# Kernel tuning notes

Measured on AMD Instinct MI355X. Metric: run time of the kernel, lower is better.

Reference implementation:

```python
import jax, jax.numpy as jnp
import numpy as np

TAU = 0.2  # temperature

def setup_inputs() -> dict:
    key = jax.random.key(0)
    k1, k2, k3 = jax.random.split(key, 3)
    query = jax.random.normal(k1, (8192, 128), dtype=jnp.float32)
    pos = jax.random.normal(k2, (8192, 128), dtype=jnp.float32)
    neg = jax.random.normal(k3, (16384, 128), dtype=jnp.float32)
    return {"query": query, "pos": pos, "neg": neg}

def reference(query, pos, neg):
    # scores: [N, M] = query @ neg^T / tau
    scores = jnp.einsum('nd,md->nm', query, neg) / TAU
    # positive logits: [N]
    pos_logit = jnp.sum(query * pos, axis=-1) / TAU
    # loss = mean_n( logsumexp_m(scores) - pos_logit )
    lse = jax.scipy.special.logsumexp(scores, axis=-1)
    return jnp.mean(lse - pos_logit)
```

## Files before the change

kernel.cpp:

```cpp
#include <hip/hip_runtime.h>
#include <cstdint>

#define NQ    8192
#define NNEG  16384
#define DIM   128
#define SPLIT 16
#define CHUNK (NNEG / SPLIT)
#define K_SCALE 7.2134752044448169f
#define LN2     0.69314718055994531f
#define EXP_C 8388608.0f
#define EXP_B 1065353216.0f

typedef __attribute__((ext_vector_type(8))) int   i32x8;
typedef __attribute__((ext_vector_type(4))) float f32x4;

union U8 { i32x8 v; int4 h[2]; };

__device__ inline void async_load16(const void* g, void* l) {
    __builtin_amdgcn_global_load_lds(
        (const __attribute__((address_space(1))) void*)g,
        (__attribute__((address_space(3))) void*)l, 16, 0, 0);
}

__device__ inline float waveReduceSum(float v) {
#pragma unroll
    for (int m = 32; m >= 1; m >>= 1) v += __shfl_xor(v, m, 64);
    return v;
}

__device__ inline float fexp2(float y, float t) {
    float v = fmaxf(fmaf(y, EXP_C, t), 0.0f);
    return __int_as_float((int)v);
}

__global__ __launch_bounds__(256) void iw_prep(
    const float* __restrict__ q, const float* __restrict__ p,
    const float* __restrict__ neg,
    unsigned char* __restrict__ qb8, unsigned char* __restrict__ nb8,
    float* __restrict__ out)
{
    const int tid = threadIdx.x;
    const int t = blockIdx.x * 256 + tid;
    constexpr int QT = NQ * DIM / 8;
    if (t < QT) {
        const float4* q4 = (const float4*)q;
        float4 v0 = q4[t * 2], v1 = q4[t * 2 + 1];
        int w0 = __builtin_amdgcn_cvt_pk_fp8_f32(v0.x * K_SCALE, v0.y * K_SCALE, 0, false);
        w0     = __builtin_amdgcn_cvt_pk_fp8_f32(v0.z * K_SCALE, v0.w * K_SCALE, w0, true);
        int w1 = __builtin_amdgcn_cvt_pk_fp8_f32(v1.x * K_SCALE, v1.y * K_SCALE, 0, false);
        w1     = __builtin_amdgcn_cvt_pk_fp8_f32(v1.z * K_SCALE, v1.w * K_SCALE, w1, true);
        ((int2*)qb8)[t] = make_int2(w0, w1);
        const float4* p4 = (const float4*)p;
        float4 p0 = p4[t * 2], p1 = p4[t * 2 + 1];
        float acc = fmaf(v0.x, p0.x, fmaf(v0.y, p0.y, fmaf(v0.z, p0.z, v0.w * p0.w)));
        acc = fmaf(v1.x, p1.x, fmaf(v1.y, p1.y, fmaf(v1.z, p1.z, fmaf(v1.w, p1.w, acc))));
        acc = waveReduceSum(acc);
        __shared__ float red[4];
        if ((tid & 63) == 0) red[tid >> 6] = acc;
        __syncthreads();
        if (tid == 0) {
            float s = red[0] + red[1] + red[2] + red[3];
            atomicAdd(out, s * (-1.0f / (0.2f * (float)NQ)));
        }
    } else {
        int j = t - QT;
        const float4* n4 = (const float4*)neg;
        float4 v0 = n4[j * 2], v1 = n4[j * 2 + 1];
        int w0 = __builtin_amdgcn_cvt_pk_fp8_f32(v0.x, v0.y, 0, false);
        w0     = __builtin_amdgcn_cvt_pk_fp8_f32(v0.z, v0.w, w0, true);
        int w1 = __builtin_amdgcn_cvt_pk_fp8_f32(v1.x, v1.y, 0, false);
        w1     = __builtin_amdgcn_cvt_pk_fp8_f32(v1.z, v1.w, w1, true);
        ((int2*)nb8)[j] = make_int2(w0, w1);
    }
}

__global__ __launch_bounds__(256, 4) void iw_main(
    const unsigned char* __restrict__ qb8, const unsigned char* __restrict__ nb8,
    float2* __restrict__ partial)
{
    constexpr int BM = 128, BN = 64, NIT = CHUNK / BN;
    __shared__ alignas(16) unsigned char n_lds[2 * BN * DIM];

    const int tid  = threadIdx.x;
    const int lane = tid & 63;
    const int w    = tid >> 6;
    const int quad = lane >> 4;
    const int c0   = lane & 15;

    const int row0   = blockIdx.x * BM;
    const int nbase0 = blockIdx.y * CHUNK;

    U8 afrag[2];
#pragma unroll
    for (int rs = 0; rs < 2; ++rs) {
        const int qrow = row0 + w * 32 + rs * 16 + c0;
        const int4* pa = reinterpret_cast<const int4*>(qb8 + (size_t)qrow * DIM + quad * 32);
        afrag[rs].h[0] = pa[0];
        afrag[rs].h[1] = pa[1];
    }

    int srcoff[2], dstoff[2];
#pragma unroll
    for (int j = 0; j < 2; ++j) {
        int L  = (w * 2 + j) * 64 + lane;
        int h  = L & 1, G = L >> 1;
        int r  = G >> 2;
        int kb = (G & 3) ^ (r & 3);
        srcoff[j] = r * DIM + kb * 32 + h * 16;
        dstoff[j] = (w * 2 + j) * 1024;
    }
#pragma unroll
    for (int j = 0; j < 2; ++j)
        async_load16(nb8 + (size_t)nbase0 * DIM + srcoff[j], n_lds + dstoff[j]);
    __syncthreads();

    const int bbase = ((c0 << 2) + (quad ^ (c0 & 3))) * 32;

    float m_s[2][4], l_s[2][4];
#pragma unroll
    for (int rs = 0; rs < 2; ++rs)
#pragma unroll
        for (int i = 0; i < 4; ++i) { m_s[rs][i] = -1e30f; l_s[rs][i] = 0.f; }

    const f32x4 zero4 = {0.f, 0.f, 0.f, 0.f};

    for (int it = 0; it < NIT; ++it) {
        const int buf = (it & 1) * (BN * DIM);
        if (it + 1 < NIT) {
            const unsigned char* src = nb8 + (size_t)(nbase0 + (it + 1) * BN) * DIM;
            const int nbuf = ((it + 1) & 1) * (BN * DIM);
#pragma unroll
            for (int j = 0; j < 2; ++j)
                async_load16(src + srcoff[j], n_lds + nbuf + dstoff[j]);
        }

        f32x4 acc[2][4];
#pragma unroll
        for (int ns = 0; ns < 4; ++ns) {
            const int4* pb = reinterpret_cast<const int4*>(n_lds + buf + bbase + ns * 2048);
            U8 b;
            b.h[0] = pb[0];
            b.h[1] = pb[1];
            acc[0][ns] = __builtin_amdgcn_mfma_scale_f32_16x16x128_f8f6f4(
                afrag[0].v, b.v, zero4, 0, 0, 0, 127, 0, 127);
            acc[1][ns] = __builtin_amdgcn_mfma_scale_f32_16x16x128_f8f6f4(
                afrag[1].v, b.v, zero4, 0, 0, 0, 127, 0, 127);
        }

#pragma unroll
        for (int rs = 0; rs < 2; ++rs) {
#pragma unroll
            for (int i = 0; i < 4; ++i) {
                float y0 = acc[rs][0][i], y1 = acc[rs][1][i];
                float y2 = acc[rs][2][i], y3 = acc[rs][3][i];
                float m0 = m_s[rs][i];
                float nm = fmaxf(fmaxf(fmaxf(y2, y3), m0), fmaxf(y0, y1));
                float t  = fmaf(nm, -EXP_C, EXP_B);
                float e0 = fexp2(y0, t), e1 = fexp2(y1, t);
                float e2 = fexp2(y2, t), e3 = fexp2(y3, t);
                float er = fexp2(m0, t);
                l_s[rs][i] = fmaf(l_s[rs][i], er, (e0 + e1) + (e2 + e3));
                m_s[rs][i] = nm;
            }
        }
        __syncthreads();
    }

#pragma unroll
    for (int rs = 0; rs < 2; ++rs) {
#pragma unroll
        for (int i = 0; i < 4; ++i) {
            float m = m_s[rs][i], l = l_s[rs][i];
#pragma unroll
            for (int s = 1; s < 16; s <<= 1) {
                float om = __shfl_xor(m, s, 64);
                float ol = __shfl_xor(l, s, 64);
                float nm = fmaxf(m, om);
                l = l * __builtin_amdgcn_exp2f(m - nm) + ol * __builtin_amdgcn_exp2f(om - nm);
                m = nm;
            }
            if (c0 == 0) {
                int grow = row0 + w * 32 + rs * 16 + quad * 4 + i;
                partial[(size_t)blockIdx.y * NQ + grow] = make_float2(m, l);
            }
        }
    }
}

__global__ __launch_bounds__(256) void iw_merge(
    const float2* __restrict__ partial, float* __restrict__ out)
{
    const int tid = threadIdx.x;
    const int row = blockIdx.x * 256 + tid;
    float M = -1e30f, L = 0.f;
#pragma unroll
    for (int c = 0; c < SPLIT; ++c) {
        float2 p = partial[(size_t)c * NQ + row];
        float nm = fmaxf(M, p.x);
        L = L * __builtin_amdgcn_exp2f(M - nm) + p.y * __builtin_amdgcn_exp2f(p.x - nm);
        M = nm;
    }
    float lse = LN2 * (M + __log2f(L));
    float v = lse * (1.0f / (float)NQ);
    v = waveReduceSum(v);
    __shared__ float red[4];
    if ((tid & 63) == 0) red[tid >> 6] = v;
    __syncthreads();
    if (tid == 0) atomicAdd(out, red[0] + red[1] + red[2] + red[3]);
}

extern "C" void kernel_launch(void* const* d_in, const int* in_sizes, int n_in,
                              void* d_out, int out_size, void* d_ws, size_t ws_size,
                              hipStream_t stream) {
    const float* q   = (const float*)d_in[0];
    const float* pos = (const float*)d_in[1];
    const float* neg = (const float*)d_in[2];
    float* out = (float*)d_out;

    unsigned char* qb8 = (unsigned char*)d_ws;
    unsigned char* nb8 = qb8 + (size_t)NQ * DIM;
    float2* partial    = (float2*)(nb8 + (size_t)NNEG * DIM);

    hipMemsetAsync(out, 0, sizeof(float), stream);
    iw_prep <<<1536, 256, 0, stream>>>(q, pos, neg, qb8, nb8, out);
    iw_main <<<dim3(NQ / 128, SPLIT), 256, 0, stream>>>(qb8, nb8, partial);
    iw_merge<<<32,   256, 0, stream>>>(partial, out);
}
```

Measured before the change: 112.7 us.

## Software-pipeline MFMA tiles with online-softmax update of previous tile

Restructures the main loop so the MFMA for tile i+1 is issued before the exp/logsumexp update of tile i, using two accumulator sets in a manually unrolled by-two loop. The goal is to overlap matrix-core latency with VALU exponent work instead of stalling on MFMA results each iteration. It raises register pressure (two accumulator arrays) under a 4-waves occupancy bound and hardcodes the iteration count (16 tiles).

Result: slower. 157.7 us (+39.9%).

```diff
diff --git a/kernel.cpp b/kernel.cpp
--- a/kernel.cpp
+++ b/kernel.cpp
@@ -124,20 +124,18 @@
 
     const f32x4 zero4 = {0.f, 0.f, 0.f, 0.f};
 
-    for (int it = 0; it < NIT; ++it) {
-        const int buf = (it & 1) * (BN * DIM);
-        if (it + 1 < NIT) {
-            const unsigned char* src = nb8 + (size_t)(nbase0 + (it + 1) * BN) * DIM;
-            const int nbuf = ((it + 1) & 1) * (BN * DIM);
-#pragma unroll
-            for (int j = 0; j < 2; ++j)
-                async_load16(src + srcoff[j], n_lds + nbuf + dstoff[j]);
-        }
-
-        f32x4 acc[2][4];
+    auto prefetch = [&](int it) {
+        const unsigned char* src = nb8 + (size_t)(nbase0 + it * BN) * DIM;
+        const int nbuf = (it & 1) * (BN * DIM);
+#pragma unroll
+        for (int j = 0; j < 2; ++j)
+            async_load16(src + srcoff[j], n_lds + nbuf + dstoff[j]);
+    };
+
+    auto compute_tile = [&](int bufoff, f32x4 (&acc)[2][4]) {
 #pragma unroll
         for (int ns = 0; ns < 4; ++ns) {
-            const int4* pb = reinterpret_cast<const int4*>(n_lds + buf + bbase + ns * 2048);
+            const int4* pb = reinterpret_cast<const int4*>(n_lds + bufoff + bbase + ns * 2048);
             U8 b;
             b.h[0] = pb[0];
             b.h[1] = pb[1];
@@ -146,7 +144,9 @@
             acc[1][ns] = __builtin_amdgcn_mfma_scale_f32_16x16x128_f8f6f4(
                 afrag[1].v, b.v, zero4, 0, 0, 0, 127, 0, 127);
         }
-
+    };
+
+    auto lse_update = [&](f32x4 (&acc)[2][4]) {
 #pragma unroll
         for (int rs = 0; rs < 2; ++rs) {
 #pragma unroll
@@ -163,8 +163,30 @@
                 m_s[rs][i] = nm;
             }
         }
+    };
+
+    f32x4 accA[2][4], accB[2][4];
+
+    prefetch(1);
+    compute_tile(0, accA);
+    __syncthreads();
+
+    for (int p = 0; p < 7; ++p) {
+        const int it = 1 + 2 * p;
+        prefetch(it + 1);
+        compute_tile(BN * DIM, accB);
+        lse_update(accA);
         __syncthreads();
-    }
+
+        prefetch(it + 2);
+        compute_tile(0, accA);
+        lse_update(accB);
+        __syncthreads();
+    }
+
+    compute_tile(BN * DIM, accB);
+    lse_update(accA);
+    lse_update(accB);
 
 #pragma unroll
     for (int rs = 0; rs < 2; ++rs) {
```

## Load negative fragments directly from global into registers with double buffering

Applied to the files above, without the earlier changes.

Removes the LDS staging buffer and async global-to-LDS loads for the negative tile. Each wave now loads its B fragments straight from global memory into registers, ping-ponging between two register sets across a manually unrolled loop, and the per-iteration block barrier is gone. Occupancy hint drops from 4 to 3 blocks to make room for the extra registers. The trade is less cross-wave sharing of B data, since each of the four waves fetches the same tile separately and relies on cache, and possible stalls from global latency.

Result: slower. 138.3 us (+22.7%).

```diff
diff --git a/kernel.cpp b/kernel.cpp
--- a/kernel.cpp
+++ b/kernel.cpp
@@ -15,12 +15,6 @@
 typedef __attribute__((ext_vector_type(4))) float f32x4;
 
 union U8 { i32x8 v; int4 h[2]; };
-
-__device__ inline void async_load16(const void* g, void* l) {
-    __builtin_amdgcn_global_load_lds(
-        (const __attribute__((address_space(1))) void*)g,
-        (__attribute__((address_space(3))) void*)l, 16, 0, 0);
-}
 
 __device__ inline float waveReduceSum(float v) {
 #pragma unroll
@@ -74,12 +68,11 @@
     }
 }
 
-__global__ __launch_bounds__(256, 4) void iw_main(
+__global__ __launch_bounds__(256, 3) void iw_main(
     const unsigned char* __restrict__ qb8, const unsigned char* __restrict__ nb8,
     float2* __restrict__ partial)
 {
-    constexpr int BM = 128, BN = 64, NIT = CHUNK / BN;
-    __shared__ alignas(16) unsigned char n_lds[2 * BN * DIM];
+    constexpr int BM = 128, BN = 64;
 
     const int tid  = threadIdx.x;
     const int lane = tid & 63;
@@ -99,22 +92,7 @@
         afrag[rs].h[1] = pa[1];
     }
 
-    int srcoff[2], dstoff[2];
-#pragma unroll
-    for (int j = 0; j < 2; ++j) {
-        int L  = (w * 2 + j) * 64 + lane;
-        int h  = L & 1, G = L >> 1;
-        int r  = G >> 2;
-        int kb = (G & 3) ^ (r & 3);
-        srcoff[j] = r * DIM + kb * 32 + h * 16;
-        dstoff[j] = (w * 2 + j) * 1024;
-    }
-#pragma unroll
-    for (int j = 0; j < 2; ++j)
-        async_load16(nb8 + (size_t)nbase0 * DIM + srcoff[j], n_lds + dstoff[j]);
-    __syncthreads();
-
-    const int bbase = ((c0 << 2) + (quad ^ (c0 & 3))) * 32;
+    const unsigned char* pt = nb8 + (size_t)(nbase0 + c0) * DIM + quad * 32;
 
     float m_s[2][4], l_s[2][4];
 #pragma unroll
@@ -123,48 +101,79 @@
         for (int i = 0; i < 4; ++i) { m_s[rs][i] = -1e30f; l_s[rs][i] = 0.f; }
 
     const f32x4 zero4 = {0.f, 0.f, 0.f, 0.f};
-
-    for (int it = 0; it < NIT; ++it) {
-        const int buf = (it & 1) * (BN * DIM);
-        if (it + 1 < NIT) {
-            const unsigned char* src = nb8 + (size_t)(nbase0 + (it + 1) * BN) * DIM;
-            const int nbuf = ((it + 1) & 1) * (BN * DIM);
-#pragma unroll
-            for (int j = 0; j < 2; ++j)
-                async_load16(src + srcoff[j], n_lds + nbuf + dstoff[j]);
-        }
-
-        f32x4 acc[2][4];
-#pragma unroll
-        for (int ns = 0; ns < 4; ++ns) {
-            const int4* pb = reinterpret_cast<const int4*>(n_lds + buf + bbase + ns * 2048);
-            U8 b;
-            b.h[0] = pb[0];
-            b.h[1] = pb[1];
-            acc[0][ns] = __builtin_amdgcn_mfma_scale_f32_16x16x128_f8f6f4(
-                afrag[0].v, b.v, zero4, 0, 0, 0, 127, 0, 127);
-            acc[1][ns] = __builtin_amdgcn_mfma_scale_f32_16x16x128_f8f6f4(
-                afrag[1].v, b.v, zero4, 0, 0, 0, 127, 0, 127);
-        }
-
-#pragma unroll
-        for (int rs = 0; rs < 2; ++rs) {
-#pragma unroll
-            for (int i = 0; i < 4; ++i) {
-                float y0 = acc[rs][0][i], y1 = acc[rs][1][i];
-                float y2 = acc[rs][2][i], y3 = acc[rs][3][i];
-                float m0 = m_s[rs][i];
-                float nm = fmaxf(fmaxf(fmaxf(y2, y3), m0), fmaxf(y0, y1));
-                float t  = fmaf(nm, -EXP_C, EXP_B);
-                float e0 = fexp2(y0, t), e1 = fexp2(y1, t);
-                float e2 = fexp2(y2, t), e3 = fexp2(y3, t);
-                float er = fexp2(m0, t);
-                l_s[rs][i] = fmaf(l_s[rs][i], er, (e0 + e1) + (e2 + e3));
-                m_s[rs][i] = nm;
-            }
-        }
-        __syncthreads();
-    }
+    f32x4 acc[2][4];
+    U8 bA[4], bB[4];
+
+#define LOADB(B, PT) do {                                                   \
+    const int4* _p0 = reinterpret_cast<const int4*>((PT));                  \
+    (B)[0].h[0] = _p0[0]; (B)[0].h[1] = _p0[1];                             \
+    const int4* _p1 = reinterpret_cast<const int4*>((PT) + 2048);           \
+    (B)[1].h[0] = _p1[0]; (B)[1].h[1] = _p1[1];                             \
+    const int4* _p2 = reinterpret_cast<const int4*>((PT) + 4096);           \
+    (B)[2].h[0] = _p2[0]; (B)[2].h[1] = _p2[1];                             \
+    const int4* _p3 = reinterpret_cast<const int4*>((PT) + 6144);           \
+    (B)[3].h[0] = _p3[0]; (B)[3].h[1] = _p3[1];                             \
+} while (0)
+
+#define COMPUTE(B) do {                                                     \
+    acc[0][0] = __builtin_amdgcn_mfma_scale_f32_16x16x128_f8f6f4(           \
+        afrag[0].v, (B)[0].v, zero4, 0, 0, 0, 127, 0, 127);                 \
+    acc[1][0] = __builtin_amdgcn_mfma_scale_f32_16x16x128_f8f6f4(           \
+        afrag[1].v, (B)[0].v, zero4, 0, 0, 0, 127, 0, 127);                 \
+    acc[0][1] = __builtin_amdgcn_mfma_scale_f32_16x16x128_f8f6f4(           \
+        afrag[0].v, (B)[1].v, zero4, 0, 0, 0, 127, 0, 127);                 \
+    acc[1][1] = __builtin_amdgcn_mfma_scale_f32_16x16x128_f8f6f4(           \
+        afrag[1].v, (B)[1].v, zero4, 0, 0, 0, 127, 0, 127);                 \
+    acc[0][2] = __builtin_amdgcn_mfma_scale_f32_16x16x128_f8f6f4(           \
+        afrag[0].v, (B)[2].v, zero4, 0, 0, 0, 127, 0, 127);                 \
+    acc[1][2] = __builtin_amdgcn_mfma_scale_f32_16x16x128_f8f6f4(           \
+        afrag[1].v, (B)[2].v, zero4, 0, 0, 0, 127, 0, 127);                 \
+    acc[0][3] = __builtin_amdgcn_mfma_scale_f32_16x16x128_f8f6f4(           \
+        afrag[0].v, (B)[3].v, zero4, 0, 0, 0, 127, 0, 127);                 \
+    acc[1][3] = __builtin_amdgcn_mfma_scale_f32_16x16x128_f8f6f4(           \
+        afrag[1].v, (B)[3].v, zero4, 0, 0, 0, 127, 0, 127);                 \
+} while (0)
+
+#define LSE_UPDATE() do {                                                   \
+    _Pragma("unroll")                                                       \
+    for (int rs = 0; rs < 2; ++rs) {                                        \
+        _Pragma("unroll")                                                   \
+        for (int i = 0; i < 4; ++i) {                                       \
+            float y0 = acc[rs][0][i], y1 = acc[rs][1][i];                   \
+            float y2 = acc[rs][2][i], y3 = acc[rs][3][i];                   \
+            float m0 = m_s[rs][i];                                          \
+            float nm = fmaxf(fmaxf(fmaxf(y2, y3), m0), fmaxf(y0, y1));      \
+            float tt = fmaf(nm, -EXP_C, EXP_B);                             \
+            float e0 = fexp2(y0, tt), e1 = fexp2(y1, tt);                   \
+            float e2 = fexp2(y2, tt), e3 = fexp2(y3, tt);                   \
+            float er = fexp2(m0, tt);                                       \
+            l_s[rs][i] = fmaf(l_s[rs][i], er, (e0 + e1) + (e2 + e3));       \
+            m_s[rs][i] = nm;                                                \
+        }                                                                   \
+    }                                                                       \
+} while (0)
+
+    LOADB(bA, pt);
+    pt += 8192;
+
+    for (int p = 0; p < 7; ++p) {
+        LOADB(bB, pt);  pt += 8192;
+        COMPUTE(bA);
+        LSE_UPDATE();
+        LOADB(bA, pt);  pt += 8192;
+        COMPUTE(bB);
+        LSE_UPDATE();
+    }
+
+    LOADB(bB, pt);
+    COMPUTE(bA);
+    LSE_UPDATE();
+    COMPUTE(bB);
+    LSE_UPDATE();
+
+#undef LOADB
+#undef COMPUTE
+#undef LSE_UPDATE
 
 #pragma unroll
     for (int rs = 0; rs < 2; ++rs) {
```

## Halve row tile and software-pipeline MFMA with online logsumexp update

Applied to the files above, without the earlier changes.

The query row tile per block shrinks from 128 to 64, so each wave holds one 16-row A fragment, and the grid doubles to 2048 blocks. The main loop is manually unrolled with two accumulator sets, so the MFMAs for tile t+1 are issued before the exp/max logsumexp update of tile t, overlapping matrix and vector work. Launch bounds drop from 4 to 2 waves per SIMD hint. Every negative tile is now loaded from LDS and global memory twice as often per query row, which raises load traffic, and register pressure from the two accumulator sets may cut occupancy.

Measured after the change: 111.4 us. About the same (-1.2%).

```diff
diff --git a/kernel.cpp b/kernel.cpp
--- a/kernel.cpp
+++ b/kernel.cpp
@@ -74,11 +74,11 @@
     }
 }
 
-__global__ __launch_bounds__(256, 4) void iw_main(
+__global__ __launch_bounds__(256, 2) void iw_main(
     const unsigned char* __restrict__ qb8, const unsigned char* __restrict__ nb8,
     float2* __restrict__ partial)
 {
-    constexpr int BM = 128, BN = 64, NIT = CHUNK / BN;
+    constexpr int BM = 64, BN = 64;
     __shared__ alignas(16) unsigned char n_lds[2 * BN * DIM];
 
     const int tid  = threadIdx.x;
@@ -90,13 +90,12 @@
     const int row0   = blockIdx.x * BM;
     const int nbase0 = blockIdx.y * CHUNK;
 
-    U8 afrag[2];
-#pragma unroll
-    for (int rs = 0; rs < 2; ++rs) {
-        const int qrow = row0 + w * 32 + rs * 16 + c0;
+    U8 afrag;
+    {
+        const int qrow = row0 + w * 16 + c0;
         const int4* pa = reinterpret_cast<const int4*>(qb8 + (size_t)qrow * DIM + quad * 32);
-        afrag[rs].h[0] = pa[0];
-        afrag[rs].h[1] = pa[1];
+        afrag.h[0] = pa[0];
+        afrag.h[1] = pa[1];
     }
 
     int srcoff[2], dstoff[2];
@@ -109,80 +108,101 @@
         srcoff[j] = r * DIM + kb * 32 + h * 16;
         dstoff[j] = (w * 2 + j) * 1024;
     }
-#pragma unroll
-    for (int j = 0; j < 2; ++j)
-        async_load16(nb8 + (size_t)nbase0 * DIM + srcoff[j], n_lds + dstoff[j]);
+
+    const int bbase = ((c0 << 2) + (quad ^ (c0 & 3))) * 32;
+
+    float m_s[4], l_s[4];
+#pragma unroll
+    for (int i = 0; i < 4; ++i) { m_s[i] = -1e30f; l_s[i] = 0.f; }
+
+    const f32x4 zero4 = {0.f, 0.f, 0.f, 0.f};
+    f32x4 accA[4], accB[4];
+
+#define PREFETCH(T) do {                                                    \
+    const unsigned char* _src = nb8 + (size_t)(nbase0 + (T) * BN) * DIM;    \
+    unsigned char* _dst = n_lds + ((T) & 1) * (BN * DIM);                   \
+    async_load16(_src + srcoff[0], _dst + dstoff[0]);                       \
+    async_load16(_src + srcoff[1], _dst + dstoff[1]);                       \
+} while (0)
+
+#define COMPUTE(ACC, T) do {                                                \
+    const unsigned char* _b = n_lds + ((T) & 1) * (BN * DIM) + bbase;       \
+    U8 _b0, _b1, _b2, _b3;                                                  \
+    { const int4* _p = reinterpret_cast<const int4*>(_b);                   \
+      _b0.h[0] = _p[0]; _b0.h[1] = _p[1]; }                                 \
+    { const int4* _p = reinterpret_cast<const int4*>(_b + 2048);            \
+      _b1.h[0] = _p[0]; _b1.h[1] = _p[1]; }                                 \
+    { const int4* _p = reinterpret_cast<const int4*>(_b + 4096);            \
+      _b2.h[0] = _p[0]; _b2.h[1] = _p[1]; }                                 \
+    { const int4* _p = reinterpret_cast<const int4*>(_b + 6144);            \
+      _b3.h[0] = _p[0]; _b3.h[1] = _p[1]; }                                 \
+    (ACC)[0] = __builtin_amdgcn_mfma_scale_f32_16x16x128_f8f6f4(            \
+        afrag.v, _b0.v, zero4, 0, 0, 0, 127, 0, 127);                       \
+    (ACC)[1] = __builtin_amdgcn_mfma_scale_f32_16x16x128_f8f6f4(            \
+        afrag.v, _b1.v, zero4, 0, 0, 0, 127, 0, 127);                       \
+    (ACC)[2] = __builtin_amdgcn_mfma_scale_f32_16x16x128_f8f6f4(            \
+        afrag.v, _b2.v, zero4, 0, 0, 0, 127, 0, 127);                       \
+    (ACC)[3] = __builtin_amdgcn_mfma_scale_f32_16x16x128_f8f6f4(            \
+        afrag.v, _b3.v, zero4, 0, 0, 0, 127, 0, 127);                       \
+} while (0)
+
+#define LSE_UPDATE(ACC) do {                                                \
+    _Pragma("unroll")                                                       \
+    for (int i = 0; i < 4; ++i) {                                           \
+        float y0 = (ACC)[0][i], y1 = (ACC)[1][i];                           \
+        float y2 = (ACC)[2][i], y3 = (ACC)[3][i];                           \
+        float m0 = m_s[i];                                                  \
+        float nm = fmaxf(fmaxf(fmaxf(y2, y3), m0), fmaxf(y0, y1));          \
+        float tt = fmaf(nm, -EXP_C, EXP_B);                                 \
+        float e0 = fexp2(y0, tt), e1 = fexp2(y1, tt);                       \
+        float e2 = fexp2(y2, tt), e3 = fexp2(y3, tt);                       \
+        float er = fexp2(m0, tt);                                           \
+        l_s[i] = fmaf(l_s[i], er, (e0 + e1) + (e2 + e3));                   \
+        m_s[i] = nm;                                                        \
+    }                                                                       \
+} while (0)
+
+    PREFETCH(0);
     __syncthreads();
-
-    const int bbase = ((c0 << 2) + (quad ^ (c0 & 3))) * 32;
-
-    float m_s[2][4], l_s[2][4];
-#pragma unroll
-    for (int rs = 0; rs < 2; ++rs)
-#pragma unroll
-        for (int i = 0; i < 4; ++i) { m_s[rs][i] = -1e30f; l_s[rs][i] = 0.f; }
-
-    const f32x4 zero4 = {0.f, 0.f, 0.f, 0.f};
-
-    for (int it = 0; it < NIT; ++it) {
-        const int buf = (it & 1) * (BN * DIM);
-        if (it + 1 < NIT) {
-            const unsigned char* src = nb8 + (size_t)(nbase0 + (it + 1) * BN) * DIM;
-            const int nbuf = ((it + 1) & 1) * (BN * DIM);
-#pragma unroll
-            for (int j = 0; j < 2; ++j)
-                async_load16(src + srcoff[j], n_lds + nbuf + dstoff[j]);
+    PREFETCH(1);
+    COMPUTE(accA, 0);
+    __syncthreads();
+
+    for (int p = 0; p < 7; ++p) {
+        const int t1 = 2 * p + 1;
+        PREFETCH(t1 + 1);
+        COMPUTE(accB, t1);
+        LSE_UPDATE(accA);
+        __syncthreads();
+
+        PREFETCH(t1 + 2);
+        COMPUTE(accA, t1 + 1);
+        LSE_UPDATE(accB);
+        __syncthreads();
+    }
+
+    COMPUTE(accB, 15);
+    LSE_UPDATE(accA);
+    LSE_UPDATE(accB);
+
+#undef PREFETCH
+#undef COMPUTE
+#undef LSE_UPDATE
+
+#pragma unroll
+    for (int i = 0; i < 4; ++i) {
+        float m = m_s[i], l = l_s[i];
+#pragma unroll
+        for (int s = 1; s < 16; s <<= 1) {
+            float om = __shfl_xor(m, s, 64);
+            float ol = __shfl_xor(l, s, 64);
+            float nm = fmaxf(m, om);
+            l = l * __builtin_amdgcn_exp2f(m - nm) + ol * __builtin_amdgcn_exp2f(om - nm);
+            m = nm;
         }
-
-        f32x4 acc[2][4];
-#pragma unroll
-        for (int ns = 0; ns < 4; ++ns) {
-            const int4* pb = reinterpret_cast<const int4*>(n_lds + buf + bbase + ns * 2048);
-            U8 b;
-            b.h[0] = pb[0];
-            b.h[1] = pb[1];
-            acc[0][ns] = __builtin_amdgcn_mfma_scale_f32_16x16x128_f8f6f4(
-                afrag[0].v, b.v, zero4, 0, 0, 0, 127, 0, 127);
-            acc[1][ns] = __builtin_amdgcn_mfma_scale_f32_16x16x128_f8f6f4(
-                afrag[1].v, b.v, zero4, 0, 0, 0, 127, 0, 127);
-        }
-
-#pragma unroll
-        for (int rs = 0; rs < 2; ++rs) {
-#pragma unroll
-            for (int i = 0; i < 4; ++i) {
-                float y0 = acc[rs][0][i], y1 = acc[rs][1][i];
-                float y2 = acc[rs][2][i], y3 = acc[rs][3][i];
-                float m0 = m_s[rs][i];
-                float nm = fmaxf(fmaxf(fmaxf(y2, y3), m0), fmaxf(y0, y1));
-                float t  = fmaf(nm, -EXP_C, EXP_B);
-                float e0 = fexp2(y0, t), e1 = fexp2(y1, t);
-                float e2 = fexp2(y2, t), e3 = fexp2(y3, t);
-                float er = fexp2(m0, t);
-                l_s[rs][i] = fmaf(l_s[rs][i], er, (e0 + e1) + (e2 + e3));
-                m_s[rs][i] = nm;
-            }
-        }
-        __syncthreads();
-    }
-
-#pragma unroll
-    for (int rs = 0; rs < 2; ++rs) {
-#pragma unroll
-        for (int i = 0; i < 4; ++i) {
-            float m = m_s[rs][i], l = l_s[rs][i];
-#pragma unroll
-            for (int s = 1; s < 16; s <<= 1) {
-                float om = __shfl_xor(m, s, 64);
-                float ol = __shfl_xor(l, s, 64);
-                float nm = fmaxf(m, om);
-                l = l * __builtin_amdgcn_exp2f(m - nm) + ol * __builtin_amdgcn_exp2f(om - nm);
-                m = nm;
-            }
-            if (c0 == 0) {
-                int grow = row0 + w * 32 + rs * 16 + quad * 4 + i;
-                partial[(size_t)blockIdx.y * NQ + grow] = make_float2(m, l);
-            }
+        if (c0 == 0) {
+            int grow = row0 + w * 16 + quad * 4 + i;
+            partial[(size_t)blockIdx.y * NQ + grow] = make_float2(m, l);
         }
     }
 }
@@ -223,6 +243,6 @@
 
     hipMemsetAsync(out, 0, sizeof(float), stream);
     iw_prep <<<1536, 256, 0, stream>>>(q, pos, neg, qb8, nb8, out);
-    iw_main <<<dim3(NQ / 128, SPLIT), 256, 0, stream>>>(qb8, nb8, partial);
+    iw_main <<<dim3(NQ / 64, SPLIT), 256, 0, stream>>>(qb8, nb8, partial);
     iw_merge<<<32,   256, 0, stream>>>(partial, out);
 }
```
